# Performance work log

Hardware: AMD Instinct MI355X
Metric: run time of the kernel (lower is better)

Reference implementation:

```python
import jax, jax.numpy as jnp
import numpy as np

N_NODES = 50000
N_EDGES = 800000


def _norm(deg):
    # DGL: norm = deg^-0.5 with inf (zero-degree) replaced by 0
    return jnp.where(deg > 0, jax.lax.rsqrt(jnp.maximum(deg, 1.0)), 0.0)


def setup_inputs() -> dict:
    key = jax.random.key(0)
    ks = jax.random.split(key, 8)
    x = jax.random.normal(ks[0], (N_NODES, 128), dtype=jnp.float32)
    W1 = jax.random.normal(ks[1], (128, 128), dtype=jnp.float32) * (1.0 / np.sqrt(128))
    b1 = jnp.zeros((128,), dtype=jnp.float32)
    W2 = jax.random.normal(ks[2], (128, 8), dtype=jnp.float32) * (1.0 / np.sqrt(128))
    b2 = jnp.zeros((8,), dtype=jnp.float32)
    src = jax.random.randint(ks[3], (N_EDGES,), 0, N_NODES, dtype=jnp.int32)
    dst = jax.random.randint(ks[4], (N_EDGES,), 0, N_NODES, dtype=jnp.int32)
    graph_ids = jnp.sort(jax.random.randint(ks[5], (N_NODES,), 0, 100, dtype=jnp.int32))
    return {"x": x, "W1": W1, "b1": b1, "W2": W2, "b2": b2,
            "src": src, "dst": dst, "graph_ids": graph_ids, "num_graphs": 100}


def _graph_conv(x, W, b, src, dst, norm_src, norm_dst):
    # GraphConv norm='both': out = D_in^{-1/2} A (D_out^{-1/2} x W) + b
    h = x @ W                                   # [N, F_out]
    msg = h[src] * norm_src[src, None]          # gather + src norm, [E, F_out]
    agg = jax.ops.segment_sum(msg, dst, num_segments=x.shape[0])  # scatter-add
    return agg * norm_dst[:, None] + b


def reference(x, W1, b1, W2, b2, src, dst, graph_ids, num_graphs):
    n = x.shape[0]
    ones_e = jnp.ones((src.shape[0],), dtype=x.dtype)
    deg_out = jax.ops.segment_sum(ones_e, src, num_segments=n)
    deg_in = jax.ops.segment_sum(ones_e, dst, num_segments=n)
    norm_src = _norm(deg_out)
    norm_dst = _norm(deg_in)

    h = _graph_conv(x, W1, b1, src, dst, norm_src, norm_dst)
    h = jax.nn.relu(h)
    h = _graph_conv(h, W2, b2, src, dst, norm_src, norm_dst)

    # dgl.mean_nodes: per-graph mean of node features
    counts = jax.ops.segment_sum(jnp.ones((n,), dtype=x.dtype), graph_ids,
                                 num_segments=num_graphs)
    sums = jax.ops.segment_sum(h, graph_ids, num_segments=num_graphs)
    return sums / jnp.maximum(counts, 1.0)[:, None]
```

## Files before the change

### kernel.cpp

```cpp
#include <hip/hip_runtime.h>

#define F1 128
#define F2 8
#define CAP 64
#define RH 8192
#define ECH 16384

typedef unsigned short us8 __attribute__((ext_vector_type(8)));
typedef short b16x8 __attribute__((ext_vector_type(8)));
typedef float f32x4 __attribute__((ext_vector_type(4)));

__device__ inline unsigned short f2bf(float f) {
  unsigned u = __float_as_uint(f);
  u += 0x7FFF + ((u >> 16) & 1);
  return (unsigned short)(u >> 16);
}
__device__ inline float bf2f(unsigned short h) {
  return __uint_as_float(((unsigned)h) << 16);
}

__global__ __launch_bounds__(256) void k_hist(const int* __restrict__ src,
                                              const int* __restrict__ dst,
                                              unsigned short* __restrict__ src16,
                                              unsigned short* __restrict__ dst16,
                                              int* __restrict__ partialA,
                                              int* __restrict__ partialB,
                                              int Epad, int E, int N) {
  __shared__ int binsA[RH];
  __shared__ int binsB[RH];
  int range0 = blockIdx.x * RH;
  int c = blockIdx.y;
  int t = threadIdx.x;
  bool writer = (blockIdx.x == 0);
  for (int i = t; i < RH; i += 256) { binsA[i] = 0; binsB[i] = 0; }
  __syncthreads();
  int e0 = c * ECH, e1 = min(e0 + ECH, Epad);
  for (int base = e0 + t * 4; base < e1; base += 1024) {
    int4 a, b;
    if (base + 4 <= E) {
      a = *(const int4*)&src[base];
      b = *(const int4*)&dst[base];
    } else {
      a.x = (base + 0 < E) ? src[base + 0] : -1;
      a.y = (base + 1 < E) ? src[base + 1] : -1;
      a.z = (base + 2 < E) ? src[base + 2] : -1;
      a.w = (base + 3 < E) ? src[base + 3] : -1;
      b.x = (base + 0 < E) ? dst[base + 0] : -1;
      b.y = (base + 1 < E) ? dst[base + 1] : -1;
      b.z = (base + 2 < E) ? dst[base + 2] : -1;
      b.w = (base + 3 < E) ? dst[base + 3] : -1;
    }
    int av[4] = {a.x, a.y, a.z, a.w};
    int bv[4] = {b.x, b.y, b.z, b.w};
#pragma unroll
    for (int j = 0; j < 4; ++j) {
      int sn = av[j] - range0;
      if (av[j] >= 0 && (unsigned)sn < (unsigned)RH) atomicAdd(&binsA[sn], 1);
      int dn = bv[j] - range0;
      if (bv[j] >= 0 && (unsigned)dn < (unsigned)RH) atomicAdd(&binsB[dn], 1);
    }
    if (writer) {
      ushort4 sa, sb;
      sa.x = av[0] >= 0 ? (unsigned short)av[0] : 0xFFFF;
      sa.y = av[1] >= 0 ? (unsigned short)av[1] : 0xFFFF;
      sa.z = av[2] >= 0 ? (unsigned short)av[2] : 0xFFFF;
      sa.w = av[3] >= 0 ? (unsigned short)av[3] : 0xFFFF;
      sb.x = bv[0] >= 0 ? (unsigned short)bv[0] : 0xFFFF;
      sb.y = bv[1] >= 0 ? (unsigned short)bv[1] : 0xFFFF;
      sb.z = bv[2] >= 0 ? (unsigned short)bv[2] : 0xFFFF;
      sb.w = bv[3] >= 0 ? (unsigned short)bv[3] : 0xFFFF;
      *(ushort4*)&src16[base] = sa;
      *(ushort4*)&dst16[base] = sb;
    }
  }
  __syncthreads();
  for (int i = t; i < RH; i += 256) {
    int n = range0 + i;
    if (n < N) {
      partialA[c * N + n] = binsA[i];
      partialB[c * N + n] = binsB[i];
    }
  }
}

__global__ void k_starts(const int* __restrict__ partialA, const int* __restrict__ partialB,
                         int* __restrict__ starts, int* __restrict__ cnt,
                         float* __restrict__ norm_src, float* __restrict__ norm_dst,
                         unsigned short* __restrict__ esrc16,
                         unsigned short* __restrict__ h1n,
                         float* __restrict__ h2n,
                         float* __restrict__ out,
                         const int* __restrict__ gids,
                         float* __restrict__ rcnt,
                         const float* __restrict__ W1,
                         unsigned short* __restrict__ Wth,
                         unsigned short* __restrict__ Wtl,
                         int N, int NCH, int NG) {
  int n = blockIdx.x * 256 + threadIdx.x;
  if (n < NG * F2) out[n] = 0.f;
  if (n < NG) {
    int g = n;
    int lo = 0, hi = N;
    while (lo < hi) { int m = (lo + hi) >> 1; if (gids[m] < g) lo = m + 1; else hi = m; }
    int lb = lo;
    lo = 0; hi = N;
    while (lo < hi) { int m = (lo + hi) >> 1; if (gids[m] <= g) lo = m + 1; else hi = m; }
    rcnt[g] = 1.f / fmaxf((float)(lo - lb), 1.f);
  }
  if (n < F1 * F1) {
    int k = n >> 7, cc = n & 127;
    float v = W1[n];
    unsigned short hi = f2bf(v);
    unsigned short lo = f2bf(v - bf2f(hi));
    Wth[cc * 128 + k] = hi;
    Wtl[cc * 128 + k] = lo;
  }
  if (n < 16) {
    us8 z = {0, 0, 0, 0, 0, 0, 0, 0};
    *(us8*)&h1n[(size_t)N * 128 + n * 8] = z;
  }
  if (n < 8) h2n[(size_t)N * 8 + n] = 0.f;
  if (n < N) {
    int dout = 0;
#pragma unroll 8
    for (int c = 0; c < NCH; ++c) dout += partialA[c * N + n];
    int run = n * CAP;
#pragma unroll 8
    for (int c = 0; c < NCH; ++c) {
      starts[c * N + n] = run;
      run += partialB[c * N + n];
    }
    int din = run - n * CAP;
    int cn = min(din, CAP);
    cnt[n] = cn;
    int cp = (cn + 15) & ~15;
    for (int pos = cn; pos < cp; ++pos) esrc16[n * CAP + pos] = (unsigned short)N;
    norm_src[n] = dout > 0 ? rsqrtf((float)dout) : 0.f;
    norm_dst[n] = din > 0 ? rsqrtf((float)din) : 0.f;
  }
}

__global__ __launch_bounds__(256) void k_scatter(const unsigned short* __restrict__ src16,
                                                 const unsigned short* __restrict__ dst16,
                                                 const int* __restrict__ starts,
                                                 unsigned short* __restrict__ esrc16,
                                                 int Epad, int N, int NCH) {
  __shared__ int cur[RH];
  int range0 = ((int)blockIdx.x / NCH) * RH;
  int c = (int)blockIdx.x % NCH;
  int t = threadIdx.x;
  for (int i = t; i < RH; i += 256) {
    int n = range0 + i;
    cur[i] = (n < N) ? starts[c * N + n] : 0;
  }
  __syncthreads();
  int e0 = c * ECH, e1 = min(e0 + ECH, Epad);
  for (int base = e0 + t * 8; base < e1; base += 2048) {
    us8 a = *(const us8*)&src16[base];
    us8 b = *(const us8*)&dst16[base];
#pragma unroll
    for (int j = 0; j < 8; ++j) {
      int dn = (int)b[j] - range0;
      if ((unsigned)dn < (unsigned)RH) {
        int node = range0 + dn;
        int p = atomicAdd(&cur[dn], 1);
        if (p < (node + 1) * CAP) esrc16[p] = a[j];
      }
    }
  }
}

__global__ __launch_bounds__(256) void k_gemm1(const float* __restrict__ x,
                                               const unsigned short* __restrict__ Wth,
                                               const unsigned short* __restrict__ Wtl,
                                               const float* __restrict__ norm_src,
                                               unsigned short* __restrict__ h1n, int N) {
  __shared__ unsigned short xh[64][72], xl[64][72];
  __shared__ unsigned short wh[128][72], wl[128][72];
  int tid = threadIdx.x;
  int row0 = blockIdx.x * 64;
  int L = tid & 63;
  int wave = tid >> 6;
  int q = L >> 4, mloc = L & 15;
  int m0 = wave * 16;
  f32x4 acc[8];
#pragma unroll
  for (int t = 0; t < 8; ++t) acc[t] = (f32x4){0.f, 0.f, 0.f, 0.f};

  for (int kb = 0; kb < 2; ++kb) {
    __syncthreads();
#pragma unroll
    for (int it = 0; it < 4; ++it) {
      int flat = tid + it * 256;
      int n = flat >> 3, kg = (flat & 7) * 8;
      us8 vh = *(const us8*)&Wth[n * 128 + kb * 64 + kg];
      us8 vl = *(const us8*)&Wtl[n * 128 + kb * 64 + kg];
      *(us8*)&wh[n][kg] = vh;
      *(us8*)&wl[n][kg] = vl;
    }
#pragma unroll
    for (int it = 0; it < 4; ++it) {
      int idx = tid + it * 256;
      int r = idx >> 4, kk = (idx & 15) * 4;
      int grow = row0 + r;
      float4 v = make_float4(0.f, 0.f, 0.f, 0.f);
      if (grow < N) v = *(const float4*)&x[(size_t)grow * 128 + kb * 64 + kk];
      ushort4 h, l;
      h.x = f2bf(v.x); l.x = f2bf(v.x - bf2f(h.x));
      h.y = f2bf(v.y); l.y = f2bf(v.y - bf2f(h.y));
      h.z = f2bf(v.z); l.z = f2bf(v.z - bf2f(h.z));
      h.w = f2bf(v.w); l.w = f2bf(v.w - bf2f(h.w));
      *(ushort4*)&xh[r][kk] = h;
      *(ushort4*)&xl[r][kk] = l;
    }
    __syncthreads();
#pragma unroll
    for (int ks = 0; ks < 2; ++ks) {
      int koff = ks * 32 + q * 8;
      b16x8 ah = *(const b16x8*)&xh[m0 + mloc][koff];
      b16x8 al = *(const b16x8*)&xl[m0 + mloc][koff];
#pragma unroll
      for (int t = 0; t < 8; ++t) {
        b16x8 bh = *(const b16x8*)&wh[t * 16 + mloc][koff];
        b16x8 bl = *(const b16x8*)&wl[t * 16 + mloc][koff];
        acc[t] = __builtin_amdgcn_mfma_f32_16x16x32_bf16(ah, bh, acc[t], 0, 0, 0);
        acc[t] = __builtin_amdgcn_mfma_f32_16x16x32_bf16(ah, bl, acc[t], 0, 0, 0);
        acc[t] = __builtin_amdgcn_mfma_f32_16x16x32_bf16(al, bh, acc[t], 0, 0, 0);
      }
    }
  }
  int rows[4];
  float ns[4];
#pragma unroll
  for (int reg = 0; reg < 4; ++reg) {
    rows[reg] = row0 + m0 + q * 4 + reg;
    ns[reg] = (rows[reg] < N) ? norm_src[rows[reg]] : 0.f;
  }
#pragma unroll
  for (int t = 0; t < 8; ++t) {
    int col = t * 16 + mloc;
#pragma unroll
    for (int reg = 0; reg < 4; ++reg) {
      if (rows[reg] < N)
        h1n[(size_t)rows[reg] * 128 + col] = f2bf(acc[t][reg] * ns[reg]);
    }
  }
}

__global__ __launch_bounds__(256) void k_agg1f(const unsigned short* __restrict__ h1n,
                                               const int* __restrict__ cnt,
                                               const unsigned short* __restrict__ esrc16,
                                               const float* __restrict__ norm_dst,
                                               const float* __restrict__ norm_src,
                                               const float* __restrict__ b1,
                                               const float* __restrict__ W2,
                                               float* __restrict__ h2n, int N) {
  int tid = threadIdx.x;
  int lane = tid & 63;
  int g = lane >> 4;
  int fl = lane & 15;
  int node = (blockIdx.x * 256 + tid - lane) / 16 + g;
  if (node >= N) return;
  int cp = (cnt[node] + 15) & ~15;
  int i0 = node * CAP;
  float acc[8] = {0.f, 0.f, 0.f, 0.f, 0.f, 0.f, 0.f, 0.f};
  for (int i = 0; i < cp; i += 16) {
#pragma unroll
    for (int t4 = 0; t4 < 16; t4 += 4) {
      ushort4 ss = *(const ushort4*)&esrc16[i0 + i + t4];
      us8 v0 = *(const us8*)&h1n[(size_t)ss.x * 128 + fl * 8];
      us8 v1 = *(const us8*)&h1n[(size_t)ss.y * 128 + fl * 8];
      us8 v2 = *(const us8*)&h1n[(size_t)ss.z * 128 + fl * 8];
      us8 v3 = *(const us8*)&h1n[(size_t)ss.w * 128 + fl * 8];
#pragma unroll
      for (int j = 0; j < 8; ++j)
        acc[j] += (bf2f(v0[j]) + bf2f(v1[j])) + (bf2f(v2[j]) + bf2f(v3[j]));
    }
  }
  float nd = norm_dst[node];
  float4 bb0 = *(const float4*)&b1[fl * 8];
  float4 bb1 = *(const float4*)&b1[fl * 8 + 4];
  float r[8];
  r[0] = fmaxf(acc[0] * nd + bb0.x, 0.f);
  r[1] = fmaxf(acc[1] * nd + bb0.y, 0.f);
  r[2] = fmaxf(acc[2] * nd + bb0.z, 0.f);
  r[3] = fmaxf(acc[3] * nd + bb0.w, 0.f);
  r[4] = fmaxf(acc[4] * nd + bb1.x, 0.f);
  r[5] = fmaxf(acc[5] * nd + bb1.y, 0.f);
  r[6] = fmaxf(acc[6] * nd + bb1.z, 0.f);
  r[7] = fmaxf(acc[7] * nd + bb1.w, 0.f);
  float4 pa = make_float4(0.f, 0.f, 0.f, 0.f);
  float4 pb = make_float4(0.f, 0.f, 0.f, 0.f);
#pragma unroll
  for (int jj = 0; jj < 8; ++jj) {
    float4 wa = *(const float4*)&W2[(fl * 8 + jj) * 8];
    float4 wb = *(const float4*)&W2[(fl * 8 + jj) * 8 + 4];
    pa.x += r[jj] * wa.x; pa.y += r[jj] * wa.y;
    pa.z += r[jj] * wa.z; pa.w += r[jj] * wa.w;
    pb.x += r[jj] * wb.x; pb.y += r[jj] * wb.y;
    pb.z += r[jj] * wb.z; pb.w += r[jj] * wb.w;
  }
#pragma unroll
  for (int d = 8; d >= 1; d >>= 1) {
    pa.x += __shfl_down(pa.x, d); pa.y += __shfl_down(pa.y, d);
    pa.z += __shfl_down(pa.z, d); pa.w += __shfl_down(pa.w, d);
    pb.x += __shfl_down(pb.x, d); pb.y += __shfl_down(pb.y, d);
    pb.z += __shfl_down(pb.z, d); pb.w += __shfl_down(pb.w, d);
  }
  if (fl == 0) {
    float ns = norm_src[node];
    pa.x *= ns; pa.y *= ns; pa.z *= ns; pa.w *= ns;
    pb.x *= ns; pb.y *= ns; pb.z *= ns; pb.w *= ns;
    *(float4*)&h2n[(size_t)node * 8] = pa;
    *(float4*)&h2n[(size_t)node * 8 + 4] = pb;
  }
}

__global__ __launch_bounds__(256) void k_agg2pool(const float* __restrict__ h2n,
                                                  const int* __restrict__ cnt,
                                                  const unsigned short* __restrict__ esrc16,
                                                  const float* __restrict__ norm_dst,
                                                  const float* __restrict__ b2,
                                                  const int* __restrict__ gids,
                                                  const float* __restrict__ rcnt,
                                                  float* __restrict__ out, int N) {
  __shared__ float bins[16 * 8];
  __shared__ int sg0;
  int tid = threadIdx.x;
  if (tid < 128) bins[tid] = 0.f;
  int base = blockIdx.x * 32;
  if (tid == 0) sg0 = gids[min(base, N - 1)];
  __syncthreads();
  int node = base + (tid >> 3);
  int j = tid & 7;
  if (node < N) {
    int cp = (cnt[node] + 15) & ~15;
    int i0 = node * CAP;
    float acc = 0.f;
    for (int i = 0; i < cp; i += 8) {
      us8 ss = *(const us8*)&esrc16[i0 + i];
      acc += ((h2n[(size_t)ss[0] * 8 + j] + h2n[(size_t)ss[1] * 8 + j]) +
              (h2n[(size_t)ss[2] * 8 + j] + h2n[(size_t)ss[3] * 8 + j])) +
             ((h2n[(size_t)ss[4] * 8 + j] + h2n[(size_t)ss[5] * 8 + j]) +
              (h2n[(size_t)ss[6] * 8 + j] + h2n[(size_t)ss[7] * 8 + j]));
    }
    float r = acc * norm_dst[node] + b2[j];
    int gid = gids[node];
    int delta = gid - sg0;
    if (delta < 16) atomicAdd(&bins[delta * 8 + j], r);
    else atomicAdd(&out[gid * 8 + j], r * rcnt[gid]);
  }
  __syncthreads();
  if (tid < 128) {
    float v = bins[tid];
    if (v != 0.f) {
      int gq = sg0 + (tid >> 3);
      atomicAdd(&out[gq * 8 + (tid & 7)], v * rcnt[gq]);
    }
  }
}

extern "C" void kernel_launch(void* const* d_in, const int* in_sizes, int n_in,
                              void* d_out, int out_size, void* d_ws, size_t ws_size,
                              hipStream_t stream) {
  const float* x  = (const float*)d_in[0];
  const float* W1 = (const float*)d_in[1];
  const float* b1 = (const float*)d_in[2];
  const float* W2 = (const float*)d_in[3];
  const float* b2 = (const float*)d_in[4];
  const int* src  = (const int*)d_in[5];
  const int* dst  = (const int*)d_in[6];
  const int* gids = (const int*)d_in[7];
  int N = in_sizes[0] / F1;
  int E = in_sizes[5];
  int NG = out_size / F2;
  float* out = (float*)d_out;

  int Epad = (E + 2047) & ~2047;
  int NR  = (N + RH - 1) / RH;
  int NCH = (Epad + ECH - 1) / ECH;

  char* p = (char*)d_ws;
  auto alloc = [&](size_t bytes) -> void* {
    void* r = (void*)p;
    p += (bytes + 255) & ~(size_t)255;
    return r;
  };
  float* rcnt    = (float*)alloc((size_t)NG * 4);
  unsigned short* src16 = (unsigned short*)alloc((size_t)Epad * 2);
  unsigned short* dst16 = (unsigned short*)alloc((size_t)Epad * 2);
  int* cnt       = (int*)alloc((size_t)N * 4);
  float* norm_src = (float*)alloc((size_t)N * 4);
  float* norm_dst = (float*)alloc((size_t)N * 4);
  unsigned short* esrc16 = (unsigned short*)alloc((size_t)N * CAP * 2);
  unsigned short* h1n = (unsigned short*)alloc((size_t)(N + 1) * F1 * 2);
  float* h2n     = (float*)alloc((size_t)(N + 1) * F2 * 4);
  unsigned short* Wth = (unsigned short*)alloc((size_t)F1 * F1 * 2);
  unsigned short* Wtl = (unsigned short*)alloc((size_t)F1 * F1 * 2);
  int* partialA  = (int*)alloc((size_t)NCH * N * 4);
  int* partialB  = (int*)alloc((size_t)NCH * N * 4);
  int* starts    = (int*)alloc((size_t)NCH * N * 4);
  (void)ws_size; (void)n_in;

  k_hist<<<dim3(NR, NCH), 256, 0, stream>>>(src, dst, src16, dst16,
                                            partialA, partialB, Epad, E, N);
  k_starts<<<(N + 255) / 256, 256, 0, stream>>>(partialA, partialB, starts, cnt,
                                                norm_src, norm_dst, esrc16, h1n, h2n,
                                                out, gids, rcnt, W1, Wth, Wtl, N, NCH, NG);
  k_scatter<<<NR * NCH, 256, 0, stream>>>(src16, dst16, starts, esrc16, Epad, N, NCH);
  k_gemm1<<<(N + 63) / 64, 256, 0, stream>>>(x, Wth, Wtl, norm_src, h1n, N);
  k_agg1f<<<(N + 15) / 16, 256, 0, stream>>>(h1n, cnt, esrc16, norm_dst, norm_src, b1, W2, h2n, N);
  k_agg2pool<<<((N * 8 + 255) / 256), 256, 0, stream>>>(h2n, cnt, esrc16, norm_dst, b2,
                                                        gids, rcnt, out, N);
}
```

Before: 217.1 us.

## Split first aggregation into feature-chunked gather and separate W2 projection kernel

Replaces the fused aggregation+ReLU+W2 kernel with a gather kernel that processes 32-feature column chunks per launch slice, using 4 lanes per node and 8 outstanding row loads. This is meant to shrink the gathered working set so h1n rows stay cache-resident. A second kernel computes the 128x8 projection from a new fp32 intermediate using W2 in shared memory. This adds a large intermediate write/read, an extra launch, and repeated index reads.

```diff
diff --git a/kernel.cpp b/kernel.cpp
--- a/kernel.cpp
+++ b/kernel.cpp
@@ -247,73 +247,81 @@
   }
 }
 
-__global__ __launch_bounds__(256) void k_agg1f(const unsigned short* __restrict__ h1n,
-                                               const int* __restrict__ cnt,
-                                               const unsigned short* __restrict__ esrc16,
-                                               const float* __restrict__ norm_dst,
-                                               const float* __restrict__ norm_src,
-                                               const float* __restrict__ b1,
-                                               const float* __restrict__ W2,
-                                               float* __restrict__ h2n, int N) {
+__global__ __launch_bounds__(256) void k_aggA(const unsigned short* __restrict__ h1n,
+                                              const int* __restrict__ cnt,
+                                              const unsigned short* __restrict__ esrc16,
+                                              const float* __restrict__ norm_dst,
+                                              const float* __restrict__ b1,
+                                              float* __restrict__ h1b,
+                                              int N, int NB) {
   int tid = threadIdx.x;
+  int fc = (int)blockIdx.x / NB;
+  int b  = (int)blockIdx.x % NB;
   int lane = tid & 63;
-  int g = lane >> 4;
-  int fl = lane & 15;
-  int node = (blockIdx.x * 256 + tid - lane) / 16 + g;
+  int wave = tid >> 6;
+  int nloc = lane >> 2;
+  int sl = lane & 3;
+  int node = b * 64 + wave * 16 + nloc;
   if (node >= N) return;
   int cp = (cnt[node] + 15) & ~15;
-  int i0 = node * CAP;
+  int fb = fc * 32 + sl * 8;
+  size_t i0 = (size_t)node * CAP;
   float acc[8] = {0.f, 0.f, 0.f, 0.f, 0.f, 0.f, 0.f, 0.f};
   for (int i = 0; i < cp; i += 16) {
 #pragma unroll
-    for (int t4 = 0; t4 < 16; t4 += 4) {
-      ushort4 ss = *(const ushort4*)&esrc16[i0 + i + t4];
-      us8 v0 = *(const us8*)&h1n[(size_t)ss.x * 128 + fl * 8];
-      us8 v1 = *(const us8*)&h1n[(size_t)ss.y * 128 + fl * 8];
-      us8 v2 = *(const us8*)&h1n[(size_t)ss.z * 128 + fl * 8];
-      us8 v3 = *(const us8*)&h1n[(size_t)ss.w * 128 + fl * 8];
+    for (int h = 0; h < 16; h += 8) {
+      ushort4 sA = *(const ushort4*)&esrc16[i0 + i + h];
+      ushort4 sB = *(const ushort4*)&esrc16[i0 + i + h + 4];
+      us8 v0 = *(const us8*)&h1n[(size_t)sA.x * 128 + fb];
+      us8 v1 = *(const us8*)&h1n[(size_t)sA.y * 128 + fb];
+      us8 v2 = *(const us8*)&h1n[(size_t)sA.z * 128 + fb];
+      us8 v3 = *(const us8*)&h1n[(size_t)sA.w * 128 + fb];
+      us8 v4 = *(const us8*)&h1n[(size_t)sB.x * 128 + fb];
+      us8 v5 = *(const us8*)&h1n[(size_t)sB.y * 128 + fb];
+      us8 v6 = *(const us8*)&h1n[(size_t)sB.z * 128 + fb];
+      us8 v7 = *(const us8*)&h1n[(size_t)sB.w * 128 + fb];
 #pragma unroll
       for (int j = 0; j < 8; ++j)
-        acc[j] += (bf2f(v0[j]) + bf2f(v1[j])) + (bf2f(v2[j]) + bf2f(v3[j]));
+        acc[j] += ((bf2f(v0[j]) + bf2f(v1[j])) + (bf2f(v2[j]) + bf2f(v3[j]))) +
+                  ((bf2f(v4[j]) + bf2f(v5[j])) + (bf2f(v6[j]) + bf2f(v7[j])));
     }
   }
   float nd = norm_dst[node];
-  float4 bb0 = *(const float4*)&b1[fl * 8];
-  float4 bb1 = *(const float4*)&b1[fl * 8 + 4];
-  float r[8];
-  r[0] = fmaxf(acc[0] * nd + bb0.x, 0.f);
-  r[1] = fmaxf(acc[1] * nd + bb0.y, 0.f);
-  r[2] = fmaxf(acc[2] * nd + bb0.z, 0.f);
-  r[3] = fmaxf(acc[3] * nd + bb0.w, 0.f);
-  r[4] = fmaxf(acc[4] * nd + bb1.x, 0.f);
-  r[5] = fmaxf(acc[5] * nd + bb1.y, 0.f);
-  r[6] = fmaxf(acc[6] * nd + bb1.z, 0.f);
-  r[7] = fmaxf(acc[7] * nd + bb1.w, 0.f);
-  float4 pa = make_float4(0.f, 0.f, 0.f, 0.f);
-  float4 pb = make_float4(0.f, 0.f, 0.f, 0.f);
-#pragma unroll
-  for (int jj = 0; jj < 8; ++jj) {
-    float4 wa = *(const float4*)&W2[(fl * 8 + jj) * 8];
-    float4 wb = *(const float4*)&W2[(fl * 8 + jj) * 8 + 4];
-    pa.x += r[jj] * wa.x; pa.y += r[jj] * wa.y;
-    pa.z += r[jj] * wa.z; pa.w += r[jj] * wa.w;
-    pb.x += r[jj] * wb.x; pb.y += r[jj] * wb.y;
-    pb.z += r[jj] * wb.z; pb.w += r[jj] * wb.w;
-  }
-#pragma unroll
-  for (int d = 8; d >= 1; d >>= 1) {
-    pa.x += __shfl_down(pa.x, d); pa.y += __shfl_down(pa.y, d);
-    pa.z += __shfl_down(pa.z, d); pa.w += __shfl_down(pa.w, d);
-    pb.x += __shfl_down(pb.x, d); pb.y += __shfl_down(pb.y, d);
-    pb.z += __shfl_down(pb.z, d); pb.w += __shfl_down(pb.w, d);
-  }
-  if (fl == 0) {
-    float ns = norm_src[node];
-    pa.x *= ns; pa.y *= ns; pa.z *= ns; pa.w *= ns;
-    pb.x *= ns; pb.y *= ns; pb.z *= ns; pb.w *= ns;
-    *(float4*)&h2n[(size_t)node * 8] = pa;
-    *(float4*)&h2n[(size_t)node * 8 + 4] = pb;
-  }
+  float4 bb0 = *(const float4*)&b1[fb];
+  float4 bb1 = *(const float4*)&b1[fb + 4];
+  float4 o0, o1;
+  o0.x = fmaxf(acc[0] * nd + bb0.x, 0.f);
+  o0.y = fmaxf(acc[1] * nd + bb0.y, 0.f);
+  o0.z = fmaxf(acc[2] * nd + bb0.z, 0.f);
+  o0.w = fmaxf(acc[3] * nd + bb0.w, 0.f);
+  o1.x = fmaxf(acc[4] * nd + bb1.x, 0.f);
+  o1.y = fmaxf(acc[5] * nd + bb1.y, 0.f);
+  o1.z = fmaxf(acc[6] * nd + bb1.z, 0.f);
+  o1.w = fmaxf(acc[7] * nd + bb1.w, 0.f);
+  *(float4*)&h1b[(size_t)node * 128 + fb] = o0;
+  *(float4*)&h1b[(size_t)node * 128 + fb + 4] = o1;
+}
+
+__global__ __launch_bounds__(256) void k_aggB(const float* __restrict__ h1b,
+                                              const float* __restrict__ W2,
+                                              const float* __restrict__ norm_src,
+                                              float* __restrict__ h2n, int N) {
+  __shared__ float W2l[128 * 8];
+  int tid = threadIdx.x;
+  for (int i = tid; i < 1024; i += 256) W2l[i] = W2[i];
+  __syncthreads();
+  int g = blockIdx.x * 256 + tid;
+  int node = g >> 3, j = g & 7;
+  if (node >= N) return;
+  const float* row = h1b + (size_t)node * 128;
+  float acc = 0.f;
+#pragma unroll
+  for (int k = 0; k < 128; k += 4) {
+    float4 v = *(const float4*)&row[k];
+    acc += v.x * W2l[(k + 0) * 8 + j] + v.y * W2l[(k + 1) * 8 + j] +
+           v.z * W2l[(k + 2) * 8 + j] + v.w * W2l[(k + 3) * 8 + j];
+  }
+  h2n[g] = acc * norm_src[node];
 }
 
 __global__ __launch_bounds__(256) void k_agg2pool(const float* __restrict__ h2n,
@@ -379,6 +387,7 @@
   int Epad = (E + 2047) & ~2047;
   int NR  = (N + RH - 1) / RH;
   int NCH = (Epad + ECH - 1) / ECH;
+  int NB  = (N + 63) / 64;
 
   char* p = (char*)d_ws;
   auto alloc = [&](size_t bytes) -> void* {
@@ -394,6 +403,7 @@
   float* norm_dst = (float*)alloc((size_t)N * 4);
   unsigned short* esrc16 = (unsigned short*)alloc((size_t)N * CAP * 2);
   unsigned short* h1n = (unsigned short*)alloc((size_t)(N + 1) * F1 * 2);
+  float* h1b     = (float*)alloc((size_t)N * F1 * 4);
   float* h2n     = (float*)alloc((size_t)(N + 1) * F2 * 4);
   unsigned short* Wth = (unsigned short*)alloc((size_t)F1 * F1 * 2);
   unsigned short* Wtl = (unsigned short*)alloc((size_t)F1 * F1 * 2);
@@ -409,7 +419,8 @@
                                                 out, gids, rcnt, W1, Wth, Wtl, N, NCH, NG);
   k_scatter<<<NR * NCH, 256, 0, stream>>>(src16, dst16, starts, esrc16, Epad, N, NCH);
   k_gemm1<<<(N + 63) / 64, 256, 0, stream>>>(x, Wth, Wtl, norm_src, h1n, N);
-  k_agg1f<<<(N + 15) / 16, 256, 0, stream>>>(h1n, cnt, esrc16, norm_dst, norm_src, b1, W2, h2n, N);
+  k_aggA<<<4 * NB, 256, 0, stream>>>(h1n, cnt, esrc16, norm_dst, b1, h1b, N, NB);
+  k_aggB<<<((size_t)N * 8 + 255) / 256, 256, 0, stream>>>(h1b, W2, norm_src, h2n, N);
   k_agg2pool<<<((N * 8 + 255) / 256), 256, 0, stream>>>(h2n, cnt, esrc16, norm_dst, b2,
                                                         gids, rcnt, out, N);
 }
```

After: 219.1 us. About the same (+0.9%).
